# Kernel optimization log

Hardware: AMD Instinct MI355X
Metric: run time of the kernel (lower is better)

Reference implementation:

```python
import jax, jax.numpy as jnp
import numpy as np


def setup_inputs() -> dict:
    key = jax.random.key(0)
    k1, k2, k3 = jax.random.split(key, 3)
    N, M, D = 8192, 8192, 128
    feat = jax.random.normal(k1, (N, D), dtype=jnp.float32)
    feat2 = jax.random.normal(k2, (M, D), dtype=jnp.float32)
    labels = jax.random.randint(k3, (N,), 0, M, dtype=jnp.int64)
    temp = jnp.array(1.0, dtype=jnp.float32)
    return {"feat": feat, "feat2": feat2, "temp": temp, "labels": labels}


def reference(feat, feat2, temp, labels):
    # (same math as sqrt(sum((x[:,None]-y)**2, -1)) but without the N*M*D intermediate).
    x_sq = jnp.sum(feat * feat, axis=-1)    # [N]
    y_sq = jnp.sum(feat2 * feat2, axis=-1)  # [M]
    sq_dist = x_sq[:, None] + y_sq[None, :] - 2.0 * (feat @ feat2.T)  # [N, M]
    dist = jnp.sqrt(jnp.maximum(sq_dist, 0.0))
    logits = -temp * dist                    # [N, M]
    # Cross-entropy with mean reduction (nn.CrossEntropyLoss default)
    log_z = jax.nn.logsumexp(logits, axis=-1)                              # [N]
    picked = jnp.take_along_axis(logits, labels[:, None], axis=1)[:, 0]   # [N]
    return jnp.mean(log_z - picked)
```

## Files before the change

kernel.cpp:

```cpp
#include <hip/hip_runtime.h>
#include <hip/hip_bf16.h>
#include <stdint.h>

#define NR 8192
#define MC 8192
#define DD 128
#define MSPLIT 16
#define CPB 512
#define TILES 16
#define ROWBLK 128

typedef __attribute__((ext_vector_type(8))) short short8;
typedef __attribute__((ext_vector_type(16))) float f32x16;

__device__ __forceinline__ ushort bf16r(float f) {
    __hip_bfloat16 h = __float2bfloat16(f);
    return *(ushort*)&h;
}

__device__ __forceinline__ void gload_lds16(const void* g, void* l) {
    __builtin_amdgcn_global_load_lds(
        (const __attribute__((address_space(1))) uint32_t*)g,
        (__attribute__((address_space(3))) uint32_t*)l, 16, 0, 0);
}
__device__ __forceinline__ void gload_lds4(const void* g, void* l) {
    __builtin_amdgcn_global_load_lds(
        (const __attribute__((address_space(1))) uint32_t*)g,
        (__attribute__((address_space(3))) uint32_t*)l, 4, 0, 0);
}

__global__ __launch_bounds__(256) void prep_kernel(
    const float* __restrict__ feat, const float* __restrict__ feat2,
    const float* __restrict__ temp_p, const int* __restrict__ labels,
    ushort* __restrict__ fb, ushort* __restrict__ f2bf,
    float* __restrict__ xsq2, float* __restrict__ ysq2,
    float* __restrict__ pick, float* __restrict__ consts) {
    int b = blockIdx.x;
    if (b < 2048) {
        int row = b * 4 + (threadIdx.x >> 6);
        int l = threadIdx.x & 63;
        float temp = *temp_p;
        float c = temp * 1.4426950408889634f;
        float c2 = c * c;
        int lab = labels[row];
        float2 x = ((const float2*)(feat  + (size_t)row * DD))[l];
        float2 y = ((const float2*)(feat2 + (size_t)row * DD))[l];
        float2 z = ((const float2*)(feat2 + (size_t)lab * DD))[l];
        ushort2 ux; ux.x = bf16r(x.x); ux.y = bf16r(x.y);
        ((ushort2*)(fb + (size_t)row * DD))[l] = ux;
        float sx = x.x * x.x + x.y * x.y;
        float sy = y.x * y.x + y.y * y.y;
        float d0 = x.x - z.x, d1 = x.y - z.y;
        float sd = d0 * d0 + d1 * d1;
        #pragma unroll
        for (int off = 1; off < 64; off <<= 1) {
            sx += __shfl_xor(sx, off);
            sy += __shfl_xor(sy, off);
            sd += __shfl_xor(sd, off);
        }
        if (l == 0) {
            xsq2[row] = c2 * sx;
            ysq2[row] = c2 * sy;
            pick[row] = temp * __builtin_amdgcn_sqrtf(sd);
            if (row == 0) consts[0] = -2.0f * c2;
        }
    } else {
        int id = (b - 2048) * 256 + threadIdx.x;
        int slot = id & 63;
        int ks = (id >> 6) & 7;
        int tile = id >> 9;
        int col = tile * 32 + (slot & 31);
        int k0 = ks * 16 + (slot >> 5) * 8;
        const float* src = feat2 + (size_t)col * DD + k0;
        float4 v0 = ((const float4*)src)[0];
        float4 v1 = ((const float4*)src)[1];
        short8 o;
        o[0] = (short)bf16r(v0.x); o[1] = (short)bf16r(v0.y);
        o[2] = (short)bf16r(v0.z); o[3] = (short)bf16r(v0.w);
        o[4] = (short)bf16r(v1.x); o[5] = (short)bf16r(v1.y);
        o[6] = (short)bf16r(v1.z); o[7] = (short)bf16r(v1.w);
        ((short8*)f2bf)[id] = o;
    }
}

__global__ __launch_bounds__(256, 3) void main_kernel(
    const ushort* __restrict__ fb, const ushort* __restrict__ f2bf,
    const float* __restrict__ xsq2, const float* __restrict__ ysq2,
    const float* __restrict__ consts, float* __restrict__ spart) {
    __shared__ ushort lds[4][8 * 512];
    __shared__ float ys_lds[CPB];

    int bid = blockIdx.x;
    int cs = bid & (MSPLIT - 1);
    int rb = bid >> 4;
    int tid = threadIdx.x;
    int wave = tid >> 6, lane = tid & 63;
    int lcol = lane & 31, lhalf = lane >> 5;
    int rowbase = rb * ROWBLK + wave * 32;
    int tile0 = cs * TILES;
    float m2c2 = consts[0];

    short8 a[8];
    const ushort* ap = fb + (size_t)(rowbase + lcol) * DD + lhalf * 8;
    #pragma unroll
    for (int ks = 0; ks < 8; ++ks) a[ks] = *(const short8*)(ap + ks * 16);

    float xs2[16];
    #pragma unroll
    for (int r = 0; r < 16; ++r)
        xs2[r] = xsq2[rowbase + (r & 3) + 8 * (r >> 2) + 4 * lhalf];

    float s[16];
    #pragma unroll
    for (int r = 0; r < 16; ++r) s[r] = 0.f;

    {
        const float* ysrc = ysq2 + cs * CPB;
        gload_lds4(ysrc + wave * 64 + lane, &ys_lds[wave * 64]);
        gload_lds4(ysrc + (wave + 4) * 64 + lane, &ys_lds[(wave + 4) * 64]);
    }
    #pragma unroll
    for (int t0 = 0; t0 < 2; ++t0) {
        const ushort* g = f2bf + ((size_t)(tile0 + t0) * 8 + wave) * 512 + lane * 8;
        gload_lds16(g, &lds[t0][wave * 512]);
        gload_lds16(g + 4 * 512, &lds[t0][(wave + 4) * 512]);
    }

    #pragma unroll 1
    for (int t = 0; t < TILES; ++t) {
        if (t + 2 < TILES) {
            const ushort* g = f2bf + ((size_t)(tile0 + t + 2) * 8 + wave) * 512 + lane * 8;
            gload_lds16(g, &lds[(t + 2) & 3][wave * 512]);
            gload_lds16(g + 4 * 512, &lds[(t + 2) & 3][(wave + 4) * 512]);
            asm volatile("s_waitcnt vmcnt(4)" ::: "memory");
        } else if (t + 1 < TILES) {
            asm volatile("s_waitcnt vmcnt(2)" ::: "memory");
        } else {
            asm volatile("s_waitcnt vmcnt(0)" ::: "memory");
        }
        __builtin_amdgcn_s_barrier();

        float ys2 = ys_lds[t * 32 + lcol];
        const ushort* lb = &lds[t & 3][0];
        f32x16 acc;
        #pragma unroll
        for (int r = 0; r < 16; ++r) acc[r] = 0.f;
        #pragma unroll
        for (int ks = 0; ks < 8; ++ks) {
            short8 bf = *(const short8*)(lb + ks * 512 + lane * 8);
            acc = __builtin_amdgcn_mfma_f32_32x32x16_bf16(a[ks], bf, acc, 0, 0, 0);
        }
        #pragma unroll
        for (int r = 0; r < 16; ++r) {
            float q = fmaf(m2c2, acc[r], xs2[r] + ys2);
            q = fmaxf(q, 0.f);
            s[r] += __builtin_amdgcn_exp2f(-__builtin_amdgcn_sqrtf(q));
        }
    }

    #pragma unroll
    for (int off = 1; off <= 16; off <<= 1)
        #pragma unroll
        for (int r = 0; r < 16; ++r) s[r] += __shfl_xor(s[r], off);

    if (lcol == 0) {
        float* sp = spart + (size_t)cs * NR + rowbase;
        #pragma unroll
        for (int r = 0; r < 16; ++r)
            sp[(r & 3) + 8 * (r >> 2) + 4 * lhalf] = s[r];
    }
}

__global__ __launch_bounds__(256) void finish1_kernel(
    const float* __restrict__ spart, const float* __restrict__ pick,
    float* __restrict__ partial) {
    __shared__ float red[4];
    int row = blockIdx.x * 256 + threadIdx.x;
    float ssum = 0.f;
    #pragma unroll
    for (int ms = 0; ms < MSPLIT; ++ms) ssum += spart[(size_t)ms * NR + row];
    float v = __builtin_amdgcn_logf(ssum) * 0.6931471805599453f + pick[row];
    #pragma unroll
    for (int off = 1; off < 64; off <<= 1) v += __shfl_xor(v, off);
    if ((threadIdx.x & 63) == 0) red[threadIdx.x >> 6] = v;
    __syncthreads();
    if (threadIdx.x == 0) partial[blockIdx.x] = red[0] + red[1] + red[2] + red[3];
}

__global__ void finish2_kernel(const float* __restrict__ partial, float* __restrict__ out) {
    float v = (threadIdx.x < 32) ? partial[threadIdx.x] : 0.f;
    #pragma unroll
    for (int off = 1; off < 64; off <<= 1) v += __shfl_xor(v, off);
    if (threadIdx.x == 0) out[0] = v * (1.0f / NR);
}

extern "C" void kernel_launch(void* const* d_in, const int* in_sizes, int n_in,
                              void* d_out, int out_size, void* d_ws, size_t ws_size,
                              hipStream_t stream) {
    const float* feat   = (const float*)d_in[0];
    const float* feat2  = (const float*)d_in[1];
    const float* temp   = (const float*)d_in[2];
    const int*   labels = (const int*)d_in[3];
    float* out = (float*)d_out;

    char* ws = (char*)d_ws;
    ushort* fb    = (ushort*)ws;
    ushort* f2bf  = (ushort*)(ws + (2u << 20));
    float*  xsq2  = (float*)(ws + (4u << 20));
    float*  ysq2  = xsq2 + NR;
    float*  pick  = ysq2 + MC;
    float*  consts  = pick + NR;
    float*  partial = consts + 16;
    float*  spart = (float*)(ws + (5u << 20));

    prep_kernel<<<2560, 256, 0, stream>>>(feat, feat2, temp, labels,
                                          fb, f2bf, xsq2, ysq2, pick, consts);
    main_kernel<<<(NR / ROWBLK) * MSPLIT, 256, 0, stream>>>(fb, f2bf, xsq2, ysq2, consts, spart);
    finish1_kernel<<<NR / 256, 256, 0, stream>>>(spart, pick, partial);
    finish2_kernel<<<1, 64, 0, stream>>>(partial, out);
}
```

Before: 43.66 us.

## Use two-wave blocks with each wave computing two 32-row MFMA tiles

Halves the block to 128 threads (two waves) and gives each wave 64 rows as two 32x32 MFMA accumulators. Each B fragment read from LDS now feeds two MFMAs, which halves LDS reads per FLOP, and each wave issues four async global-to-LDS loads per tile instead of two. In exchange, per-wave register pressure roughly doubles (A fragments, accumulators, row norms, partial sums), and there are fewer waves per block to hide the latency of the sqrt/exp2 epilogue.

```diff
diff --git a/kernel.cpp b/kernel.cpp
--- a/kernel.cpp
+++ b/kernel.cpp
@@ -83,7 +83,7 @@
     }
 }
 
-__global__ __launch_bounds__(256, 3) void main_kernel(
+__global__ __launch_bounds__(128, 2) void main_kernel(
     const ushort* __restrict__ fb, const ushort* __restrict__ f2bf,
     const float* __restrict__ xsq2, const float* __restrict__ ysq2,
     const float* __restrict__ consts, float* __restrict__ spart) {
@@ -96,78 +96,100 @@
     int tid = threadIdx.x;
     int wave = tid >> 6, lane = tid & 63;
     int lcol = lane & 31, lhalf = lane >> 5;
-    int rowbase = rb * ROWBLK + wave * 32;
+    int rowbase = rb * ROWBLK + wave * 64;
     int tile0 = cs * TILES;
     float m2c2 = consts[0];
 
-    short8 a[8];
-    const ushort* ap = fb + (size_t)(rowbase + lcol) * DD + lhalf * 8;
-    #pragma unroll
-    for (int ks = 0; ks < 8; ++ks) a[ks] = *(const short8*)(ap + ks * 16);
-
-    float xs2[16];
-    #pragma unroll
-    for (int r = 0; r < 16; ++r)
-        xs2[r] = xsq2[rowbase + (r & 3) + 8 * (r >> 2) + 4 * lhalf];
-
-    float s[16];
-    #pragma unroll
-    for (int r = 0; r < 16; ++r) s[r] = 0.f;
+    short8 a[2][8];
+    #pragma unroll
+    for (int rt = 0; rt < 2; ++rt) {
+        const ushort* ap = fb + (size_t)(rowbase + rt * 32 + lcol) * DD + lhalf * 8;
+        #pragma unroll
+        for (int ks = 0; ks < 8; ++ks) a[rt][ks] = *(const short8*)(ap + ks * 16);
+    }
+
+    float xs2[2][16];
+    #pragma unroll
+    for (int rt = 0; rt < 2; ++rt)
+        #pragma unroll
+        for (int r = 0; r < 16; ++r)
+            xs2[rt][r] = xsq2[rowbase + rt * 32 + (r & 3) + 8 * (r >> 2) + 4 * lhalf];
+
+    float s[2][16];
+    #pragma unroll
+    for (int rt = 0; rt < 2; ++rt)
+        #pragma unroll
+        for (int r = 0; r < 16; ++r) s[rt][r] = 0.f;
 
     {
         const float* ysrc = ysq2 + cs * CPB;
-        gload_lds4(ysrc + wave * 64 + lane, &ys_lds[wave * 64]);
-        gload_lds4(ysrc + (wave + 4) * 64 + lane, &ys_lds[(wave + 4) * 64]);
-    }
-    #pragma unroll
-    for (int t0 = 0; t0 < 2; ++t0) {
-        const ushort* g = f2bf + ((size_t)(tile0 + t0) * 8 + wave) * 512 + lane * 8;
-        gload_lds16(g, &lds[t0][wave * 512]);
-        gload_lds16(g + 4 * 512, &lds[t0][(wave + 4) * 512]);
+        #pragma unroll
+        for (int c = 0; c < 4; ++c) {
+            int ch = wave * 4 + c;
+            gload_lds4(ysrc + ch * 64 + lane, &ys_lds[ch * 64]);
+        }
+        #pragma unroll
+        for (int t0 = 0; t0 < 2; ++t0)
+            #pragma unroll
+            for (int c = 0; c < 4; ++c) {
+                int ch = wave * 4 + c;
+                gload_lds16(f2bf + ((size_t)(tile0 + t0) * 8 + ch) * 512 + lane * 8,
+                            &lds[t0][ch * 512]);
+            }
     }
 
     #pragma unroll 1
     for (int t = 0; t < TILES; ++t) {
         if (t + 2 < TILES) {
-            const ushort* g = f2bf + ((size_t)(tile0 + t + 2) * 8 + wave) * 512 + lane * 8;
-            gload_lds16(g, &lds[(t + 2) & 3][wave * 512]);
-            gload_lds16(g + 4 * 512, &lds[(t + 2) & 3][(wave + 4) * 512]);
+            #pragma unroll
+            for (int c = 0; c < 4; ++c) {
+                int ch = wave * 4 + c;
+                gload_lds16(f2bf + ((size_t)(tile0 + t + 2) * 8 + ch) * 512 + lane * 8,
+                            &lds[(t + 2) & 3][ch * 512]);
+            }
+            asm volatile("s_waitcnt vmcnt(8)" ::: "memory");
+        } else if (t + 1 < TILES) {
             asm volatile("s_waitcnt vmcnt(4)" ::: "memory");
-        } else if (t + 1 < TILES) {
-            asm volatile("s_waitcnt vmcnt(2)" ::: "memory");
         } else {
             asm volatile("s_waitcnt vmcnt(0)" ::: "memory");
         }
         __builtin_amdgcn_s_barrier();
 
-        float ys2 = ys_lds[t * 32 + lcol];
+        float ysv = ys_lds[t * 32 + lcol];
         const ushort* lb = &lds[t & 3][0];
-        f32x16 acc;
-        #pragma unroll
-        for (int r = 0; r < 16; ++r) acc[r] = 0.f;
+        f32x16 acc0, acc1;
+        #pragma unroll
+        for (int r = 0; r < 16; ++r) { acc0[r] = 0.f; acc1[r] = 0.f; }
         #pragma unroll
         for (int ks = 0; ks < 8; ++ks) {
             short8 bf = *(const short8*)(lb + ks * 512 + lane * 8);
-            acc = __builtin_amdgcn_mfma_f32_32x32x16_bf16(a[ks], bf, acc, 0, 0, 0);
+            acc0 = __builtin_amdgcn_mfma_f32_32x32x16_bf16(a[0][ks], bf, acc0, 0, 0, 0);
+            acc1 = __builtin_amdgcn_mfma_f32_32x32x16_bf16(a[1][ks], bf, acc1, 0, 0, 0);
         }
         #pragma unroll
         for (int r = 0; r < 16; ++r) {
-            float q = fmaf(m2c2, acc[r], xs2[r] + ys2);
-            q = fmaxf(q, 0.f);
-            s[r] += __builtin_amdgcn_exp2f(-__builtin_amdgcn_sqrtf(q));
+            float q0 = fmaxf(fmaf(m2c2, acc0[r], xs2[0][r] + ysv), 0.f);
+            float q1 = fmaxf(fmaf(m2c2, acc1[r], xs2[1][r] + ysv), 0.f);
+            s[0][r] += __builtin_amdgcn_exp2f(-__builtin_amdgcn_sqrtf(q0));
+            s[1][r] += __builtin_amdgcn_exp2f(-__builtin_amdgcn_sqrtf(q1));
         }
     }
 
     #pragma unroll
     for (int off = 1; off <= 16; off <<= 1)
         #pragma unroll
-        for (int r = 0; r < 16; ++r) s[r] += __shfl_xor(s[r], off);
+        for (int rt = 0; rt < 2; ++rt)
+            #pragma unroll
+            for (int r = 0; r < 16; ++r)
+                s[rt][r] += __shfl_xor(s[rt][r], off);
 
     if (lcol == 0) {
         float* sp = spart + (size_t)cs * NR + rowbase;
         #pragma unroll
-        for (int r = 0; r < 16; ++r)
-            sp[(r & 3) + 8 * (r >> 2) + 4 * lhalf] = s[r];
+        for (int rt = 0; rt < 2; ++rt)
+            #pragma unroll
+            for (int r = 0; r < 16; ++r)
+                sp[rt * 32 + (r & 3) + 8 * (r >> 2) + 4 * lhalf] = s[rt][r];
     }
 }
 
@@ -215,7 +237,7 @@
 
     prep_kernel<<<2560, 256, 0, stream>>>(feat, feat2, temp, labels,
                                           fb, f2bf, xsq2, ysq2, pick, consts);
-    main_kernel<<<(NR / ROWBLK) * MSPLIT, 256, 0, stream>>>(fb, f2bf, xsq2, ysq2, consts, spart);
+    main_kernel<<<(NR / ROWBLK) * MSPLIT, 128, 0, stream>>>(fb, f2bf, xsq2, ysq2, consts, spart);
     finish1_kernel<<<NR / 256, 256, 0, stream>>>(spart, pick, partial);
     finish2_kernel<<<1, 64, 0, stream>>>(partial, out);
 }
```

Result: slower. 48.09 us (+10.2%).
